# Kernel tuning notes

Hardware: AMD Instinct MI355X
Metric: run time of the kernel (lower is better)

The kernel has to match this reference:

```python
import jax, jax.numpy as jnp
import numpy as np

N_GROUPS = 4


def setup_inputs() -> dict:
    key = jax.random.key(0)
    ks = jax.random.split(key, 6)
    I, J, B = 512, 512, 4  # query tokens, key tokens, grid batch (B = 1 * n_groups)
    n_dim, out_per_group = 128, 4  # n_heads // n_groups = 16 // 4
    grid_q = jax.random.normal(ks[0], (I, 3), dtype=jnp.float32)
    grid_kv = jax.random.normal(ks[1], (B, J, 3), dtype=jnp.float32)
    W1 = jax.random.normal(ks[2], (3, n_dim), dtype=jnp.float32) * (1.0 / np.sqrt(3))
    b1 = jnp.zeros((n_dim,), dtype=jnp.float32)
    W2 = jax.random.normal(ks[3], (n_dim, n_dim), dtype=jnp.float32) * (1.0 / np.sqrt(n_dim))
    b2 = jnp.zeros((n_dim,), dtype=jnp.float32)
    W3 = jax.random.normal(ks[4], (n_dim, out_per_group), dtype=jnp.float32) * (1.0 / np.sqrt(n_dim))
    b3 = jnp.zeros((out_per_group,), dtype=jnp.float32)
    return {"grid_q": grid_q, "grid_kv": grid_kv, "W1": W1, "b1": b1,
            "W2": W2, "b2": b2, "W3": W3, "b3": b3}


def reference(grid_q, grid_kv, W1, b1, W2, b2, W3, b3):
    # grid_q: [I, 3] -> [1, I, 3]; grid_kv: [B, J, 3]
    gq = grid_q[None, :, :]
    # pairwise position difference: [B, I, J, 3]
    pos = gq[:, :, None, :] - grid_kv[:, None, :, :]
    # sign-log transform
    bias = jnp.sign(pos) * jnp.log1p(jnp.abs(pos))
    # tiny MLP: 3 -> n_dim -> n_dim -> heads//groups, pointwise over (B, I, J)
    h = jax.nn.relu(jnp.einsum('bijc,cd->bijd', bias, W1) + b1)
    h = jax.nn.relu(jnp.einsum('bijd,de->bije', h, W2) + b2)
    out = jnp.einsum('bije,eo->bijo', h, W3) + b3  # [B, I, J, O]
    # rearrange '(b g) i j o -> b (g o) i j' with g = N_GROUPS
    B, I, J, O = out.shape
    out = out.reshape(B // N_GROUPS, N_GROUPS, I, J, O)
    out = jnp.transpose(out, (0, 1, 4, 2, 3)).reshape(B // N_GROUPS, N_GROUPS * O, I, J)
    return out
```

## Files before the change

### kernel.cpp

```cpp
#include <hip/hip_runtime.h>
#include <math.h>

#define NDIM 128
#define TILE 64
#define NBLOCKS 1024
#define THREADS 512
#define POS_PER_BLOCK 1024
#define ITERS 16
#define CH 512

typedef __attribute__((ext_vector_type(8)))  short  short8;
typedef __attribute__((ext_vector_type(4)))  float  float4v;
typedef __attribute__((ext_vector_type(16))) float  float16;

__device__ __forceinline__ unsigned cvt_pk(float lo, float hi) {
    unsigned r;
    asm("v_cvt_pk_bf16_f32 %0, %1, %2" : "=v"(r) : "v"(lo), "v"(hi));
    return r;
}

__device__ __forceinline__ int kmap(int c, int jj) {
    return 32 * (c >> 2) + 16 * ((c >> 1) & 1) + 4 * (c & 1) + ((jj >> 2) << 3) + (jj & 3);
}

__global__ __launch_bounds__(512, 4)
void crpb_mfma6(const float* __restrict__ gq,
                const float* __restrict__ gkv,
                const float* __restrict__ W1,
                const float* __restrict__ b1,
                const float* __restrict__ W2,
                const float* __restrict__ b2,
                const float* __restrict__ W3,
                const float* __restrict__ b3,
                float* __restrict__ out)
{
    __shared__ __align__(16) unsigned short ash[2][16 * CH];
    __shared__ __align__(16) float red[2][4 * 4 * 64];
    __shared__ __align__(16) float b2s[NDIM];

    const int tid  = threadIdx.x;
    const int lane = tid & 63;
    const int w    = __builtin_amdgcn_readfirstlane(tid >> 6);
    const int l31  = lane & 31;
    const int lh   = lane >> 5;

    if (tid < NDIM) b2s[tid] = b2[tid];

    const int ct = w & 3;
    const int ph = w >> 2;

    short8 a2f[8];
    #pragma unroll
    for (int ks = 0; ks < 8; ++ks) {
        const int c = 2 * ks + lh;
        unsigned t0[4];
        #pragma unroll
        for (int t = 0; t < 4; ++t) {
            const int d0 = kmap(c, 2 * t), d1 = d0 + 1;
            const int e0 = ct * 32 + l31;
            t0[t] = cvt_pk(W2[d0 * 128 + e0], W2[d1 * 128 + e0]);
        }
        __builtin_memcpy(&a2f[ks], t0, 16);
    }

    short8 w3a[2];
    #pragma unroll
    for (int m = 0; m < 2; ++m) {
        unsigned tt[4];
        #pragma unroll
        for (int t = 0; t < 4; ++t) {
            const int chl = ((2 * t) & 3) + 8 * ((2 * t) >> 2) + 4 * lh + 16 * m;
            const int ch0 = ct * 32 + chl, ch1 = ch0 + 1;
            const float lo = (l31 < 4) ? W3[ch0 * 4 + l31] : 0.0f;
            const float hi = (l31 < 4) ? W3[ch1 * 4 + l31] : 0.0f;
            tt[t] = cvt_pk(lo, hi);
        }
        __builtin_memcpy(&w3a[m], tt, 16);
    }
    const float b3r = b3[(tid >> 6) & 3];

    const int posblock = blockIdx.x * POS_PER_BLOCK;
    const int bb = posblock >> 18;
    const float* kvrow = gkv + (size_t)(bb << 9) * 3;

    int ii = (posblock >> 9) & 511;
    float q0 = gq[ii * 3 + 0], q1 = gq[ii * 3 + 1], q2 = gq[ii * 3 + 2];
    const float* kp = kvrow + (size_t)((posblock & 511) + lane) * 3;
    float kv0 = kp[0], kv1 = kp[1], kv2 = kp[2];

    auto phaseA = [&](int x, int buf) {
        const float c0 = q0 - kv0, c1 = q1 - kv1, c2 = q2 - kv2;
        const int pn = posblock + (((x + 1) & 15) << 6);
        const int iN = (pn >> 9) & 511, jN = pn & 511;
        q0 = gq[iN * 3 + 0]; q1 = gq[iN * 3 + 1]; q2 = gq[iN * 3 + 2];
        const float* kn = kvrow + (size_t)(jN + lane) * 3;
        kv0 = kn[0]; kv1 = kn[1]; kv2 = kn[2];

        const float f0 = copysignf(__logf(1.0f + fabsf(c0)), c0);
        const float f1 = copysignf(__logf(1.0f + fabsf(c1)), c1);
        const float f2 = copysignf(__logf(1.0f + fabsf(c2)), c2);
        #pragma unroll
        for (int u = 0; u < 2; ++u) {
            const int c = 2 * w + u;
            unsigned pk[4];
            #pragma unroll
            for (int t = 0; t < 4; ++t) {
                const int ch0 = kmap(c, 2 * t), ch1 = ch0 + 1;
                float h0 = fmaf(f2, W1[256 + ch0], fmaf(f1, W1[128 + ch0],
                           fmaf(f0, W1[ch0], b1[ch0])));
                float h1 = fmaf(f2, W1[256 + ch1], fmaf(f1, W1[128 + ch1],
                           fmaf(f0, W1[ch1], b1[ch1])));
                pk[t] = cvt_pk(fmaxf(h0, 0.0f), fmaxf(h1, 0.0f));
            }
            short8 v; __builtin_memcpy(&v, pk, 16);
            *(short8*)&ash[buf][c * CH + lane * 8] = v;
        }
    };

    phaseA(0, 0);
    __syncthreads();

    for (int it = 0; it < ITERS; ++it) {
        const int buf = it & 1;
        const int posbase = posblock + it * TILE;
        const int i  = (posbase >> 9) & 511;
        const int jb = posbase & 511;

        float16 acc;
        #pragma unroll
        for (int qr = 0; qr < 4; ++qr) {
            float4v iv = *(const float4v*)&b2s[ct * 32 + 8 * qr + 4 * lh];
            #pragma unroll
            for (int t = 0; t < 4; ++t) acc[4 * qr + t] = iv[t];
        }
        const unsigned short* br = &ash[buf][lh * CH + (ph * 32 + l31) * 8];
        #pragma unroll
        for (int ks = 0; ks < 8; ++ks) {
            short8 bfrag = *(const short8*)(br + ks * 2 * CH);
            acc = __builtin_amdgcn_mfma_f32_32x32x16_bf16(a2f[ks], bfrag, acc, 0, 0, 0);
        }

        {
            unsigned pk0[4], pk1[4];
            #pragma unroll
            for (int t = 0; t < 4; ++t) {
                pk0[t] = cvt_pk(fmaxf(acc[2 * t], 0.f),     fmaxf(acc[2 * t + 1], 0.f));
                pk1[t] = cvt_pk(fmaxf(acc[8 + 2 * t], 0.f), fmaxf(acc[8 + 2 * t + 1], 0.f));
            }
            short8 bm0, bm1;
            __builtin_memcpy(&bm0, pk0, 16);
            __builtin_memcpy(&bm1, pk1, 16);
            float16 p;
            #pragma unroll
            for (int r = 0; r < 16; ++r) p[r] = 0.0f;
            p = __builtin_amdgcn_mfma_f32_32x32x16_bf16(w3a[0], bm0, p, 0, 0, 0);
            p = __builtin_amdgcn_mfma_f32_32x32x16_bf16(w3a[1], bm1, p, 0, 0, 0);
            if (lh == 0) {
                #pragma unroll
                for (int o = 0; o < 4; ++o)
                    red[buf][(ct * 4 + o) * 64 + ph * 32 + l31] = p[o];
            }
        }

        if (it != ITERS - 1) phaseA(it + 1, 1 - buf);

        __syncthreads();

        if (tid < 256) {
            const int o = tid >> 6, pos = tid & 63;
            const float* rb = &red[buf][o * 64 + pos];
            const float v = b3r + rb[0] + rb[256] + rb[512] + rb[768];
            out[((size_t)((bb << 2) + o) << 18) + ((size_t)i << 9) + jb + pos] = v;
        }
    }
}

extern "C" void kernel_launch(void* const* d_in, const int* in_sizes, int n_in,
                              void* d_out, int out_size, void* d_ws, size_t ws_size,
                              hipStream_t stream) {
    const float* gq  = (const float*)d_in[0];
    const float* gkv = (const float*)d_in[1];
    const float* W1  = (const float*)d_in[2];
    const float* b1  = (const float*)d_in[3];
    const float* W2  = (const float*)d_in[4];
    const float* b2  = (const float*)d_in[5];
    const float* W3  = (const float*)d_in[6];
    const float* b3  = (const float*)d_in[7];
    float* out = (float*)d_out;

    crpb_mfma6<<<NBLOCKS, THREADS, 0, stream>>>(gq, gkv, W1, b1, W2, b2, W3, b3, out);
}
```

Baseline: 127.2 us.

## Compute first MLP layer with MFMA using split-bf16 operands

Replaces the per-thread scalar FMA evaluation of the 3->128 first layer with one 32x32x16 bf16 MFMA per wave. Inputs and W1 are split into high and low bf16 parts so that the cross products approximate fp32 precision. Bias vectors b1 and b2 are preloaded into registers as accumulator initial values, which removes the shared-memory b2 staging. Each wave now computes its own 32-channel slice for its position half, which changes the LDS write pattern, and register pressure rises from the extra float16 vectors.

```diff
diff --git a/kernel.cpp b/kernel.cpp
--- a/kernel.cpp
+++ b/kernel.cpp
@@ -10,7 +10,6 @@
 #define CH 512
 
 typedef __attribute__((ext_vector_type(8)))  short  short8;
-typedef __attribute__((ext_vector_type(4)))  float  float4v;
 typedef __attribute__((ext_vector_type(16))) float  float16;
 
 __device__ __forceinline__ unsigned cvt_pk(float lo, float hi) {
@@ -24,7 +23,7 @@
 }
 
 __global__ __launch_bounds__(512, 4)
-void crpb_mfma6(const float* __restrict__ gq,
+void crpb_mfma7(const float* __restrict__ gq,
                 const float* __restrict__ gkv,
                 const float* __restrict__ W1,
                 const float* __restrict__ b1,
@@ -36,7 +35,6 @@
 {
     __shared__ __align__(16) unsigned short ash[2][16 * CH];
     __shared__ __align__(16) float red[2][4 * 4 * 64];
-    __shared__ __align__(16) float b2s[NDIM];
 
     const int tid  = threadIdx.x;
     const int lane = tid & 63;
@@ -44,10 +42,38 @@
     const int l31  = lane & 31;
     const int lh   = lane >> 5;
 
-    if (tid < NDIM) b2s[tid] = b2[tid];
-
     const int ct = w & 3;
     const int ph = w >> 2;
+
+    float16 b1cv, b2cv;
+    #pragma unroll
+    for (int q = 0; q < 16; ++q) {
+        const int row = (q & 3) + 8 * (q >> 2) + 4 * lh;
+        b1cv[q] = b1[ct * 32 + row];
+        b2cv[q] = b2[ct * 32 + row];
+    }
+
+    short8 w1f;
+    {
+        const int ch = ct * 32 + l31;
+        const float w0 = W1[ch], w1v = W1[128 + ch], w2v = W1[256 + ch];
+        const unsigned u0 = cvt_pk(w0, w0), u1 = cvt_pk(w1v, w1v), u2 = cvt_pk(w2v, w2v);
+        const float w0h = __uint_as_float(u0 << 16);
+        const float w1h = __uint_as_float(u1 << 16);
+        const float w2h = __uint_as_float(u2 << 16);
+        const float w0l = w0 - w0h, w1l = w1v - w1h, w2l = w2v - w2h;
+        unsigned d[4];
+        if (lh == 0) {
+            d[0] = cvt_pk(w0h, w0l);
+            d[1] = cvt_pk(w0h, w1h);
+            d[2] = cvt_pk(w1l, w1h);
+            d[3] = cvt_pk(w2h, w2l);
+        } else {
+            d[0] = cvt_pk(w2h, 0.0f);
+            d[1] = 0; d[2] = 0; d[3] = 0;
+        }
+        __builtin_memcpy(&w1f, d, 16);
+    }
 
     short8 a2f[8];
     #pragma unroll
@@ -57,8 +83,7 @@
         #pragma unroll
         for (int t = 0; t < 4; ++t) {
             const int d0 = kmap(c, 2 * t), d1 = d0 + 1;
-            const int e0 = ct * 32 + l31;
-            t0[t] = cvt_pk(W2[d0 * 128 + e0], W2[d1 * 128 + e0]);
+            t0[t] = cvt_pk(W2[d0 * 128 + ct * 32 + l31], W2[d1 * 128 + ct * 32 + l31]);
         }
         __builtin_memcpy(&a2f[ks], t0, 16);
     }
@@ -85,7 +110,8 @@
 
     int ii = (posblock >> 9) & 511;
     float q0 = gq[ii * 3 + 0], q1 = gq[ii * 3 + 1], q2 = gq[ii * 3 + 2];
-    const float* kp = kvrow + (size_t)((posblock & 511) + lane) * 3;
+    const int pofs = ph * 32 + l31;
+    const float* kp = kvrow + (size_t)((posblock & 511) + pofs) * 3;
     float kv0 = kp[0], kv1 = kp[1], kv2 = kp[2];
 
     auto phaseA = [&](int x, int buf) {
@@ -93,28 +119,44 @@
         const int pn = posblock + (((x + 1) & 15) << 6);
         const int iN = (pn >> 9) & 511, jN = pn & 511;
         q0 = gq[iN * 3 + 0]; q1 = gq[iN * 3 + 1]; q2 = gq[iN * 3 + 2];
-        const float* kn = kvrow + (size_t)(jN + lane) * 3;
+        const float* kn = kvrow + (size_t)(jN + pofs) * 3;
         kv0 = kn[0]; kv1 = kn[1]; kv2 = kn[2];
 
         const float f0 = copysignf(__logf(1.0f + fabsf(c0)), c0);
         const float f1 = copysignf(__logf(1.0f + fabsf(c1)), c1);
         const float f2 = copysignf(__logf(1.0f + fabsf(c2)), c2);
-        #pragma unroll
-        for (int u = 0; u < 2; ++u) {
-            const int c = 2 * w + u;
-            unsigned pk[4];
-            #pragma unroll
-            for (int t = 0; t < 4; ++t) {
-                const int ch0 = kmap(c, 2 * t), ch1 = ch0 + 1;
-                float h0 = fmaf(f2, W1[256 + ch0], fmaf(f1, W1[128 + ch0],
-                           fmaf(f0, W1[ch0], b1[ch0])));
-                float h1 = fmaf(f2, W1[256 + ch1], fmaf(f1, W1[128 + ch1],
-                           fmaf(f0, W1[ch1], b1[ch1])));
-                pk[t] = cvt_pk(fmaxf(h0, 0.0f), fmaxf(h1, 0.0f));
-            }
-            short8 v; __builtin_memcpy(&v, pk, 16);
-            *(short8*)&ash[buf][c * CH + lane * 8] = v;
-        }
+
+        const unsigned u0 = cvt_pk(f0, f0), u1 = cvt_pk(f1, f1), u2 = cvt_pk(f2, f2);
+        const float f0h = __uint_as_float(u0 << 16);
+        const float f1h = __uint_as_float(u1 << 16);
+        const float f2h = __uint_as_float(u2 << 16);
+        const float f0l = f0 - f0h, f1l = f1 - f1h, f2l = f2 - f2h;
+
+        unsigned d[4];
+        if (lh == 0) {
+            d[0] = u0;
+            d[1] = cvt_pk(f0l, f1);
+            d[2] = cvt_pk(f1, f1l);
+            d[3] = u2;
+        } else {
+            d[0] = cvt_pk(f2l, 0.0f);
+            d[1] = 0; d[2] = 0; d[3] = 0;
+        }
+        short8 bf; __builtin_memcpy(&bf, d, 16);
+
+        float16 c1r = __builtin_amdgcn_mfma_f32_32x32x16_bf16(w1f, bf, b1cv, 0, 0, 0);
+
+        unsigned pk0[4], pk1[4];
+        #pragma unroll
+        for (int t = 0; t < 4; ++t) {
+            pk0[t] = cvt_pk(fmaxf(c1r[2 * t], 0.f),     fmaxf(c1r[2 * t + 1], 0.f));
+            pk1[t] = cvt_pk(fmaxf(c1r[8 + 2 * t], 0.f), fmaxf(c1r[8 + 2 * t + 1], 0.f));
+        }
+        short8 v0, v1;
+        __builtin_memcpy(&v0, pk0, 16);
+        __builtin_memcpy(&v1, pk1, 16);
+        *(short8*)&ash[buf][(4 * ct + lh) * CH + pofs * 8]     = v0;
+        *(short8*)&ash[buf][(4 * ct + 2 + lh) * CH + pofs * 8] = v1;
     };
 
     phaseA(0, 0);
@@ -126,16 +168,11 @@
         const int i  = (posbase >> 9) & 511;
         const int jb = posbase & 511;
 
-        float16 acc;
-        #pragma unroll
-        for (int qr = 0; qr < 4; ++qr) {
-            float4v iv = *(const float4v*)&b2s[ct * 32 + 8 * qr + 4 * lh];
-            #pragma unroll
-            for (int t = 0; t < 4; ++t) acc[4 * qr + t] = iv[t];
-        }
         const unsigned short* br = &ash[buf][lh * CH + (ph * 32 + l31) * 8];
-        #pragma unroll
-        for (int ks = 0; ks < 8; ++ks) {
+        short8 bfrag0 = *(const short8*)(br);
+        float16 acc = __builtin_amdgcn_mfma_f32_32x32x16_bf16(a2f[0], bfrag0, b2cv, 0, 0, 0);
+        #pragma unroll
+        for (int ks = 1; ks < 8; ++ks) {
             short8 bfrag = *(const short8*)(br + ks * 2 * CH);
             acc = __builtin_amdgcn_mfma_f32_32x32x16_bf16(a2f[ks], bfrag, acc, 0, 0, 0);
         }
@@ -188,5 +225,5 @@
     const float* b3  = (const float*)d_in[7];
     float* out = (float*)d_out;
 
-    crpb_mfma6<<<NBLOCKS, THREADS, 0, stream>>>(gq, gkv, W1, b1, W2, b2, W3, b3, out);
-}
+    crpb_mfma7<<<NBLOCKS, THREADS, 0, stream>>>(gq, gkv, W1, b1, W2, b2, W3, b3, out);
+}
```

New measurement: 125.7 us. Within noise of the previous version (-1.2%).
